# Kernel optimization log

Hardware: AMD Instinct MI355X
Metric: run time of the kernel (lower is better)

The kernel has to match this reference:

```python
import jax, jax.numpy as jnp
import numpy as np

V, N = 3, 32768
C2, C3 = 256, 32          # feat_ch_2D, feat_ch_3D
H = W = 128               # 2D feature map size
D = 32                    # 3D volume feature size
CIN = C2 + C3             # 288, MLP in_channels


def setup_inputs() -> dict:
    key = jax.random.key(0)
    ks = jax.random.split(key, 16)
    sc = 0.02
    inp = {
        'pts': jax.random.uniform(ks[0], (1, N, 3), minval=-0.5, maxval=0.5),
        'pts_proj': jax.random.uniform(ks[1], (1, N, 2), minval=-1.0, maxval=1.0),
        'img_feat0': jax.random.normal(ks[2], (V, C2, H, W)),
        'img_feat1': jax.random.normal(ks[3], (V, C2, H, W)),
        'vol_feat0': jax.random.normal(ks[4], (V, C3, D, D, D)),
        'vol_feat1': jax.random.normal(ks[5], (V, C3, D, D, D)),
        'W0': jax.random.normal(ks[6], (1024, CIN)) * sc,  'b0': jnp.zeros((1024,)),
        'W1': jax.random.normal(ks[7], (512, CIN + 1024)) * sc, 'b1': jnp.zeros((512,)),
        'W2': jax.random.normal(ks[8], (256, CIN + 512)) * sc,  'b2': jnp.zeros((256,)),
        'W3': jax.random.normal(ks[9], (128, CIN + 256)) * sc,  'b3': jnp.zeros((128,)),
        'W4': jax.random.normal(ks[10], (1, 128)) * sc,         'b4': jnp.zeros((1,)),
        'mean_num': 3,
    }
    return inp


def _gs2d(feat, gx, gy):
    # feat: [C,H,W]; gx,gy: [N] normalized coords in [-1,1]
    C, Hh, Ww = feat.shape
    ix = jnp.clip(((gx + 1.0) * Ww - 1.0) * 0.5, 0.0, Ww - 1.0)  # align_corners=False, border pad
    iy = jnp.clip(((gy + 1.0) * Hh - 1.0) * 0.5, 0.0, Hh - 1.0)
    x0f, y0f = jnp.floor(ix), jnp.floor(iy)
    wx, wy = ix - x0f, iy - y0f
    x0 = x0f.astype(jnp.int32); x1 = jnp.minimum(x0 + 1, Ww - 1)
    y0 = y0f.astype(jnp.int32); y1 = jnp.minimum(y0 + 1, Hh - 1)
    v00 = feat[:, y0, x0]; v01 = feat[:, y0, x1]
    v10 = feat[:, y1, x0]; v11 = feat[:, y1, x1]
    return (v00 * (1 - wy) * (1 - wx) + v01 * (1 - wy) * wx
            + v10 * wy * (1 - wx) + v11 * wy * wx)  # [C,N]


def _gs3d(feat, gx, gy, gz):
    # feat: [C,D,H,W]; grid x->W, y->H, z->D (torch grid_sample convention)
    C, Dd, Hh, Ww = feat.shape
    ix = jnp.clip(((gx + 1.0) * Ww - 1.0) * 0.5, 0.0, Ww - 1.0)
    iy = jnp.clip(((gy + 1.0) * Hh - 1.0) * 0.5, 0.0, Hh - 1.0)
    iz = jnp.clip(((gz + 1.0) * Dd - 1.0) * 0.5, 0.0, Dd - 1.0)
    x0f, y0f, z0f = jnp.floor(ix), jnp.floor(iy), jnp.floor(iz)
    wx, wy, wz = ix - x0f, iy - y0f, iz - z0f
    x0 = x0f.astype(jnp.int32); x1 = jnp.minimum(x0 + 1, Ww - 1)
    y0 = y0f.astype(jnp.int32); y1 = jnp.minimum(y0 + 1, Hh - 1)
    z0 = z0f.astype(jnp.int32); z1 = jnp.minimum(z0 + 1, Dd - 1)
    def g(zi, yi, xi):
        return feat[:, zi, yi, xi]  # [C,N]
    out = (g(z0, y0, x0) * (1 - wz) * (1 - wy) * (1 - wx)
           + g(z0, y0, x1) * (1 - wz) * (1 - wy) * wx
           + g(z0, y1, x0) * (1 - wz) * wy * (1 - wx)
           + g(z0, y1, x1) * (1 - wz) * wy * wx
           + g(z1, y0, x0) * wz * (1 - wy) * (1 - wx)
           + g(z1, y0, x1) * wz * (1 - wy) * wx
           + g(z1, y1, x0) * wz * wy * (1 - wx)
           + g(z1, y1, x1) * wz * wy * wx)
    return out  # [C,N]


def _lrelu(x):
    return jnp.where(x >= 0, x, 0.2 * x)


def _conv1x1(Wm, bm, x):
    # x: [V,C,N] -> [V,O,N]
    return jnp.einsum('oc,vcn->von', Wm, x) + bm[None, :, None]


def _mlp0(x, W0, b0, W1, b1, W2, b2, W3, b3):
    out = _lrelu(_conv1x1(W0, b0, x))
    out = _lrelu(_conv1x1(W1, b1, jnp.concatenate([x, out], axis=1)))
    out = _lrelu(_conv1x1(W2, b2, jnp.concatenate([x, out], axis=1)))
    out = _lrelu(_conv1x1(W3, b3, jnp.concatenate([x, out], axis=1)))
    return out  # [V,128,N]


def _forward(pts, pts_proj, img_feats, vol_feats,
             W0, b0, W1, b1, W2, b2, W3, b3, W4, b4, mean_num):
    v = img_feats[0].shape[0]
    gx2 = jnp.broadcast_to(pts_proj[:, :, 0], (v, pts_proj.shape[1]))
    gy2 = jnp.broadcast_to(pts_proj[:, :, 1], (v, pts_proj.shape[1]))
    p = pts * 2.0  # pts *= 2.0 before 3D sampling
    gx3 = jnp.broadcast_to(p[:, :, 0], (v, p.shape[1]))
    gy3 = jnp.broadcast_to(p[:, :, 1], (v, p.shape[1]))
    gz3 = jnp.broadcast_to(p[:, :, 2], (v, p.shape[1]))
    outs = []
    for img_feat, vol_feat in zip(img_feats, vol_feats):
        f2 = jax.vmap(_gs2d)(img_feat, gx2, gy2)            # [V,C2,N]
        f3 = jax.vmap(_gs3d)(vol_feat, gx3, gy3, gz3)       # [V,C3,N]
        pt_feat = jnp.concatenate([f2, f3], axis=1)         # [V,288,N]
        pt_out0 = _mlp0(pt_feat, W0, b0, W1, b1, W2, b2, W3, b3)
        pt_out0_mean = jnp.mean(pt_out0[:mean_num], axis=0, keepdims=True)  # [1,128,N]
        sdf = jax.nn.sigmoid(_conv1x1(W4, b4, pt_out0_mean))                # [1,1,N]
        outs.append(jnp.transpose(sdf, (0, 2, 1)))                          # [1,N,1]
    return tuple(outs)


def reference(pts, pts_proj, img_feat0, img_feat1, vol_feat0, vol_feat1,
              W0, b0, W1, b1, W2, b2, W3, b3, W4, b4, mean_num):
    return _forward(pts, pts_proj, [img_feat0, img_feat1], [vol_feat0, vol_feat1],
                    W0, b0, W1, b1, W2, b2, W3, b3, W4, b4, mean_num)
```

## Files before the change

kernel.cpp:

```cpp
#include <hip/hip_runtime.h>
#include <hip/hip_bf16.h>

#define NV 3
#define NPTS 32768
#define C2C 256
#define C3C 32
#define CINC 288
#define CINP 320
#define HH 128
#define WWW 128
#define DDD 32

typedef short bh8 __attribute__((ext_vector_type(8)));
typedef float fx4 __attribute__((ext_vector_type(4)));
typedef unsigned short us4 __attribute__((ext_vector_type(4)));

__device__ __forceinline__ float b2f(unsigned short u) {
    unsigned int x = ((unsigned int)u) << 16;
    return __uint_as_float(x);
}
__device__ __forceinline__ unsigned short f2b(float f) {
    unsigned int x = __float_as_uint(f);
    unsigned int r = (x + 0x7FFFu + ((x >> 16) & 1u)) >> 16;
    return (unsigned short)r;
}

__device__ __forceinline__ void gl2lds16(const unsigned short* g, unsigned short* l) {
    __builtin_amdgcn_global_load_lds(
        (const __attribute__((address_space(1))) unsigned int*)g,
        (__attribute__((address_space(3))) unsigned int*)l, 16, 0, 0);
}

__device__ __forceinline__ int xcd_swz(int orig, int nwg) {
    int xcd = orig & 7;
    int q = nwg >> 3, r = nwg & 7;
    int base = (xcd < r) ? xcd * (q + 1) : r * (q + 1) + (xcd - r) * q;
    return base + (orig >> 3);
}

__global__ void k_wpad(const float* __restrict__ src, unsigned short* __restrict__ dst, int M, int Kp) {
    int idx = blockIdx.x * 256 + threadIdx.x;
    if (idx >= M * Kp) return;
    int m = idx / Kp, k = idx - m * Kp;
    int Ksrc = Kp - 32;
    float v;
    if (k < CINC) v = src[(size_t)m * Ksrc + k];
    else if (k < CINP) v = 0.0f;
    else v = src[(size_t)m * Ksrc + (k - 32)];
    dst[idx] = f2b(v);
}

__global__ void k_timg(const float* __restrict__ in, unsigned short* __restrict__ out) {
    int v = blockIdx.x >> 7, y = blockIdx.x & 127;
    int x0 = blockIdx.y << 6, c0 = blockIdx.z << 6;
    __shared__ float t[64][65];
    int tx = threadIdx.x & 63, tg = threadIdx.x >> 6;
    const float* src = in + (((size_t)(v * C2C + c0) * HH + y) * WWW + x0);
#pragma unroll
    for (int i = 0; i < 16; i++) {
        int cl = tg * 16 + i;
        t[cl][tx] = src[(size_t)cl * (HH * WWW) + tx];
    }
    __syncthreads();
    unsigned short* dst = out + ((size_t)(v * HH + y) * WWW + x0) * C2C + c0;
#pragma unroll
    for (int i = 0; i < 16; i++) {
        int xl = tg * 16 + i;
        dst[(size_t)xl * C2C + tx] = f2b(t[tx][xl]);
    }
}

__global__ void k_tvol(const float* __restrict__ in, unsigned short* __restrict__ out) {
    int v = blockIdx.x;
    int s0 = blockIdx.y << 8;
    __shared__ float t[32][257];
    int tid = threadIdx.x;
    const float* src = in + (size_t)v * C3C * 32768 + s0;
#pragma unroll
    for (int c = 0; c < 32; c++) t[c][tid] = src[(size_t)c * 32768 + tid];
    __syncthreads();
    unsigned short* dst = out + ((size_t)v * 32768 + s0) * C3C;
    int c = tid & 31, sb = tid >> 5;
#pragma unroll
    for (int j = 0; j < 32; j++) {
        int sl = j * 8 + sb;
        dst[(size_t)sl * C3C + c] = f2b(t[c][sl]);
    }
}

__global__ __launch_bounds__(256) void k_sample(const float* __restrict__ pts, const float* __restrict__ proj,
                         const unsigned short* __restrict__ imgT, const unsigned short* __restrict__ volT,
                         unsigned short* __restrict__ ptT, int n0, int Nk) {
    int w = threadIdx.x >> 6, l = threadIdx.x & 63;
    int i = blockIdx.x * 4 + w;
    int v = blockIdx.y;
    int n = n0 + i;
    unsigned short* dstRow = ptT + (size_t)(v * Nk + i) * CINP;

    {
        float gx = proj[n * 2 + 0], gy = proj[n * 2 + 1];
        float ix = fminf(fmaxf(((gx + 1.0f) * (float)WWW - 1.0f) * 0.5f, 0.0f), (float)(WWW - 1));
        float iy = fminf(fmaxf(((gy + 1.0f) * (float)HH - 1.0f) * 0.5f, 0.0f), (float)(HH - 1));
        float x0f = floorf(ix), y0f = floorf(iy);
        float wx = ix - x0f, wy = iy - y0f;
        int x0 = (int)x0f, y0 = (int)y0f;
        int x1 = min(x0 + 1, WWW - 1), y1 = min(y0 + 1, HH - 1);
        const unsigned short* base = imgT + (size_t)v * HH * WWW * C2C;
        us4 a = *((const us4*)(base + ((size_t)(y0 * WWW + x0)) * C2C) + l);
        us4 b = *((const us4*)(base + ((size_t)(y0 * WWW + x1)) * C2C) + l);
        us4 c = *((const us4*)(base + ((size_t)(y1 * WWW + x0)) * C2C) + l);
        us4 d = *((const us4*)(base + ((size_t)(y1 * WWW + x1)) * C2C) + l);
        float w00 = (1.0f - wy) * (1.0f - wx), w01 = (1.0f - wy) * wx;
        float w10 = wy * (1.0f - wx), w11 = wy * wx;
        us4 rv;
#pragma unroll
        for (int r = 0; r < 4; r++) {
            float f = b2f(a[r]) * w00 + b2f(b[r]) * w01 + b2f(c[r]) * w10 + b2f(d[r]) * w11;
            rv[r] = f2b(f);
        }
        *(us4*)(dstRow + l * 4) = rv;
    }
    {
        float gx = pts[n * 3 + 0] * 2.0f, gy = pts[n * 3 + 1] * 2.0f, gz = pts[n * 3 + 2] * 2.0f;
        float ix = fminf(fmaxf(((gx + 1.0f) * (float)DDD - 1.0f) * 0.5f, 0.0f), (float)(DDD - 1));
        float iy = fminf(fmaxf(((gy + 1.0f) * (float)DDD - 1.0f) * 0.5f, 0.0f), (float)(DDD - 1));
        float iz = fminf(fmaxf(((gz + 1.0f) * (float)DDD - 1.0f) * 0.5f, 0.0f), (float)(DDD - 1));
        float x0f = floorf(ix), y0f = floorf(iy), z0f = floorf(iz);
        float wx = ix - x0f, wy = iy - y0f, wz = iz - z0f;
        int x0 = (int)x0f, y0 = (int)y0f, z0 = (int)z0f;
        int x1 = min(x0 + 1, DDD - 1), y1 = min(y0 + 1, DDD - 1), z1 = min(z0 + 1, DDD - 1);
        int c = l & 31, zs = l >> 5;
        int zi = zs ? z1 : z0;
        float wzs = zs ? wz : (1.0f - wz);
        const unsigned short* base = volT + (size_t)v * 32768 * C3C;
        float f00 = b2f(base[((size_t)((zi * 32 + y0) * 32 + x0)) * C3C + c]);
        float f01 = b2f(base[((size_t)((zi * 32 + y0) * 32 + x1)) * C3C + c]);
        float f10 = b2f(base[((size_t)((zi * 32 + y1) * 32 + x0)) * C3C + c]);
        float f11 = b2f(base[((size_t)((zi * 32 + y1) * 32 + x1)) * C3C + c]);
        float r = (f00 * (1.0f - wy) * (1.0f - wx) + f01 * (1.0f - wy) * wx +
                   f10 * wy * (1.0f - wx) + f11 * wy * wx) * wzs;
        float other = __shfl_xor(r, 32);
        r += other;
        if (zs == 0) dstRow[C2C + c] = f2b(r);
    }
    if (l < 8) *(us4*)(dstRow + CINC + l * 4) = (us4){0, 0, 0, 0};
}

template <int K1, int K2, int M>
__device__ __forceinline__ void gemm128_body(const unsigned short* __restrict__ A,
                                             const unsigned short* __restrict__ B1,
                                             const unsigned short* __restrict__ B2,
                                             const float* __restrict__ bias,
                                             unsigned short* __restrict__ C) {
    constexpr int K = K1 + K2;
    __shared__ unsigned short Ash[128 * 32];
    __shared__ unsigned short Bsh[128 * 32];
    int tid = threadIdx.x;
    int w = tid >> 6, l = tid & 63;
    int la = l & 15, lg = l >> 4;
    int wm = w & 1, wn = w >> 1;
    int gx = gridDim.x;
    int nwg = gx * gridDim.y;
    int bid = xcd_swz(blockIdx.y * gx + blockIdx.x, nwg);
    int mBlk = (bid % gx) * 128;
    int nBlk = (bid / gx) * 128;

    int sRow = l >> 2;
    int sCol = (l & 3) * 8;

    fx4 acc[4][4];
#pragma unroll
    for (int mi = 0; mi < 4; mi++)
#pragma unroll
        for (int ni = 0; ni < 4; ni++) acc[mi][ni] = (fx4){0.f, 0.f, 0.f, 0.f};

    const unsigned short* Ag = A + (size_t)mBlk * K;
    {
        const unsigned short* Bg = B1 + (size_t)nBlk * K1;
        for (int k0 = 0; k0 < K1; k0 += 32) {
#pragma unroll
            for (int j = 0; j < 2; j++) {
                int r = w * 32 + j * 16 + sRow;
                gl2lds16(Ag + (size_t)r * K + k0 + sCol, &Ash[r * 32 + sCol]);
                gl2lds16(Bg + (size_t)r * K1 + k0 + sCol, &Bsh[r * 32 + sCol]);
            }
            __syncthreads();
            bh8 af[4], bfv[4];
#pragma unroll
            for (int mi = 0; mi < 4; mi++) af[mi] = *(const bh8*)&Ash[(wm * 64 + mi * 16 + la) * 32 + lg * 8];
#pragma unroll
            for (int ni = 0; ni < 4; ni++) bfv[ni] = *(const bh8*)&Bsh[(wn * 64 + ni * 16 + la) * 32 + lg * 8];
#pragma unroll
            for (int mi = 0; mi < 4; mi++)
#pragma unroll
                for (int ni = 0; ni < 4; ni++)
                    acc[mi][ni] = __builtin_amdgcn_mfma_f32_16x16x32_bf16(af[mi], bfv[ni], acc[mi][ni], 0, 0, 0);
            __syncthreads();
        }
    }
    if constexpr (K2 > 0) {
        const unsigned short* Bg = B2 + (size_t)nBlk * K2;
        for (int k0 = 0; k0 < K2; k0 += 32) {
#pragma unroll
            for (int j = 0; j < 2; j++) {
                int r = w * 32 + j * 16 + sRow;
                gl2lds16(Ag + (size_t)r * K + K1 + k0 + sCol, &Ash[r * 32 + sCol]);
                gl2lds16(Bg + (size_t)r * K2 + k0 + sCol, &Bsh[r * 32 + sCol]);
            }
            __syncthreads();
            bh8 af[4], bfv[4];
#pragma unroll
            for (int mi = 0; mi < 4; mi++) af[mi] = *(const bh8*)&Ash[(wm * 64 + mi * 16 + la) * 32 + lg * 8];
#pragma unroll
            for (int ni = 0; ni < 4; ni++) bfv[ni] = *(const bh8*)&Bsh[(wn * 64 + ni * 16 + la) * 32 + lg * 8];
#pragma unroll
            for (int mi = 0; mi < 4; mi++)
#pragma unroll
                for (int ni = 0; ni < 4; ni++)
                    acc[mi][ni] = __builtin_amdgcn_mfma_f32_16x16x32_bf16(af[mi], bfv[ni], acc[mi][ni], 0, 0, 0);
            __syncthreads();
        }
    }

#pragma unroll
    for (int mi = 0; mi < 4; mi++) {
        int m0 = mBlk + wm * 64 + mi * 16 + lg * 4;
        fx4 bb = *(const fx4*)(bias + m0);
#pragma unroll
        for (int ni = 0; ni < 4; ni++) {
            int n = nBlk + wn * 64 + ni * 16 + la;
            us4 rv;
#pragma unroll
            for (int r = 0; r < 4; r++) {
                float x = acc[mi][ni][r] + bb[r];
                x = (x >= 0.0f) ? x : 0.2f * x;
                rv[r] = f2b(x);
            }
            *(us4*)(C + (size_t)n * M + m0) = rv;
        }
    }
}

__global__ __launch_bounds__(256) void k_g0(const unsigned short* __restrict__ A, const unsigned short* __restrict__ B1,
                                            const float* __restrict__ bias, unsigned short* __restrict__ C) {
    gemm128_body<320, 0, 1024>(A, B1, nullptr, bias, C);
}
__global__ __launch_bounds__(256) void k_g2(const unsigned short* __restrict__ A, const unsigned short* __restrict__ B1,
                                            const unsigned short* __restrict__ B2, const float* __restrict__ bias,
                                            unsigned short* __restrict__ C) {
    gemm128_body<320, 512, 256>(A, B1, B2, bias, C);
}
__global__ __launch_bounds__(256) void k_g3(const unsigned short* __restrict__ A, const unsigned short* __restrict__ B1,
                                            const unsigned short* __restrict__ B2, const float* __restrict__ bias,
                                            unsigned short* __restrict__ C) {
    gemm128_body<320, 256, 128>(A, B1, B2, bias, C);
}

__global__ __launch_bounds__(512) void k_g1(const unsigned short* __restrict__ A,
                                            const unsigned short* __restrict__ B1,
                                            const unsigned short* __restrict__ B2,
                                            const float* __restrict__ bias,
                                            unsigned short* __restrict__ C, int nOff) {
    constexpr int Kp = 1344;
    constexpr int K2 = 1024;
    constexpr int M = 512;
    constexpr int nt = Kp >> 6;
    __shared__ unsigned short As[2][256 * 64];
    __shared__ unsigned short Bs[2][256 * 64];
    int tid = threadIdx.x;
    int w = tid >> 6, l = tid & 63;
    int la = l & 15, lg = l >> 4;
    int wm = w >> 2, wn = w & 3;
    int gx = gridDim.x;
    int nwg = gx * gridDim.y;
    int bid = xcd_swz(blockIdx.y * gx + blockIdx.x, nwg);
    int mBlk = (bid % gx) * 256;
    int nBlk = (bid / gx) * 256 + nOff;

    const unsigned short* Ag = A + (size_t)mBlk * Kp;

    fx4 acc[8][4];
#pragma unroll
    for (int mi = 0; mi < 8; mi++)
#pragma unroll
        for (int ni = 0; ni < 4; ni++) acc[mi][ni] = (fx4){0.f, 0.f, 0.f, 0.f};

    auto burst = [&](int t, int nxt) {
        const unsigned short* bsrc;
        size_t ldb;
        int kc;
        if (t < 5) { bsrc = B1; ldb = CINP; kc = t * 64; }
        else       { bsrc = B2; ldb = (size_t)K2; kc = (t - 5) * 64; }
        bsrc += (size_t)nBlk * ldb + kc;
        const unsigned short* asrc = Ag + t * 64;
#pragma unroll
        for (int h = 0; h < 2; h++)
#pragma unroll
            for (int j = 0; j < 2; j++) {
                int idx = j * 512 + tid;
                int r = (h << 7) + (idx >> 3);
                int c = (idx & 7) ^ (r & 7);
                gl2lds16(asrc + (size_t)r * Kp + c * 8, &As[nxt][(h << 13) + idx * 8]);
            }
#pragma unroll
        for (int h = 0; h < 2; h++)
#pragma unroll
            for (int j = 0; j < 2; j++) {
                int idx = j * 512 + tid;
                int r = (h << 7) + (idx >> 3);
                int c = (idx & 7) ^ (r & 7);
                gl2lds16(bsrc + (size_t)r * ldb + c * 8, &Bs[nxt][(h << 13) + idx * 8]);
            }
    };

    burst(0, 0);
    asm volatile("s_waitcnt vmcnt(0)" ::: "memory");
    __builtin_amdgcn_s_barrier();
    for (int t = 0; t < nt; t++) {
        int cur = t & 1;
        const unsigned short* Ab = &As[cur][0];
        const unsigned short* Bb = &Bs[cur][0];
        bh8 afr[4][2];
#pragma unroll
        for (int p = 0; p < 4; p++) {
            int qm = p >> 1, qn = p & 1;
            if (qn == 0) {
#pragma unroll
                for (int m2 = 0; m2 < 4; m2++)
#pragma unroll
                    for (int s = 0; s < 2; s++) {
                        int row = wm * 128 + (qm * 4 + m2) * 16 + la;
                        int c = (s * 4 + lg) ^ (row & 7);
                        afr[m2][s] = *(const bh8*)&Ab[row * 64 + c * 8];
                    }
            }
            bh8 bfr[2][2];
#pragma unroll
            for (int n2 = 0; n2 < 2; n2++)
#pragma unroll
                for (int s = 0; s < 2; s++) {
                    int row = wn * 64 + (qn * 2 + n2) * 16 + la;
                    int c = (s * 4 + lg) ^ (row & 7);
                    bfr[n2][s] = *(const bh8*)&Bb[row * 64 + c * 8];
                }
            __builtin_amdgcn_s_barrier();
            __builtin_amdgcn_s_setprio(1);
#pragma unroll
            for (int m2 = 0; m2 < 4; m2++)
#pragma unroll
                for (int n2 = 0; n2 < 2; n2++)
#pragma unroll
                    for (int s = 0; s < 2; s++)
                        acc[qm * 4 + m2][qn * 2 + n2] = __builtin_amdgcn_mfma_f32_16x16x32_bf16(
                            afr[m2][s], bfr[n2][s], acc[qm * 4 + m2][qn * 2 + n2], 0, 0, 0);
            __builtin_amdgcn_s_setprio(0);
            if (p == 0 && t + 1 < nt) burst(t + 1, cur ^ 1);
            if (p == 3) {
                asm volatile("s_waitcnt lgkmcnt(0)" ::: "memory");
                if (t + 1 < nt) asm volatile("s_waitcnt vmcnt(8)" ::: "memory");
            }
            __builtin_amdgcn_s_barrier();
        }
    }

#pragma unroll
    for (int mi = 0; mi < 8; mi++) {
        int m0 = mBlk + wm * 128 + mi * 16 + lg * 4;
        fx4 bb = *(const fx4*)(bias + m0);
#pragma unroll
        for (int ni = 0; ni < 4; ni++) {
            int n = nBlk + wn * 64 + ni * 16 + la;
            us4 rv;
#pragma unroll
            for (int r = 0; r < 4; r++) {
                float x = acc[mi][ni][r] + bb[r];
                x = (x >= 0.0f) ? x : 0.2f * x;
                rv[r] = f2b(x);
            }
            *(us4*)(C + (size_t)n * M + m0) = rv;
        }
    }
}

__global__ __launch_bounds__(256) void k_head(const unsigned short* __restrict__ o3, const float* __restrict__ W4,
                       const float* __restrict__ b4, const int* __restrict__ mn_p,
                       float* __restrict__ out, int n0, int Nk, int level) {
    int wv = threadIdx.x >> 6, l = threadIdx.x & 63;
    int sub = l >> 4, cl = l & 15;
    int i = blockIdx.x * 16 + wv * 4 + sub;
    if (i >= Nk) return;
    int mn = *mn_p;
    if (mn > NV) mn = NV;
    if (mn < 1) mn = 1;
    fx4 w0 = *(const fx4*)(W4 + cl * 8);
    fx4 w1 = *(const fx4*)(W4 + cl * 8 + 4);
    float s = 0.0f;
    for (int v = 0; v < mn; v++) {
        bh8 x = *(const bh8*)(o3 + (size_t)(v * Nk + i) * 128 + cl * 8);
#pragma unroll
        for (int r = 0; r < 4; r++) s += w0[r] * b2f((unsigned short)x[r]);
#pragma unroll
        for (int r = 0; r < 4; r++) s += w1[r] * b2f((unsigned short)x[4 + r]);
    }
#pragma unroll
    for (int m = 1; m < 16; m <<= 1) s += __shfl_xor(s, m);
    if (cl == 0) {
        s = s / (float)mn + b4[0];
        out[(size_t)level * NPTS + n0 + i] = 1.0f / (1.0f + expf(-s));
    }
}

extern "C" void kernel_launch(void* const* d_in, const int* in_sizes, int n_in,
                              void* d_out, int out_size, void* d_ws, size_t ws_size,
                              hipStream_t stream) {
    const float* pts = (const float*)d_in[0];
    const float* proj = (const float*)d_in[1];
    const float* img[2] = {(const float*)d_in[2], (const float*)d_in[3]};
    const float* vol[2] = {(const float*)d_in[4], (const float*)d_in[5]};
    const float* Wf[4] = {(const float*)d_in[6], (const float*)d_in[8], (const float*)d_in[10], (const float*)d_in[12]};
    const float* bf[4] = {(const float*)d_in[7], (const float*)d_in[9], (const float*)d_in[11], (const float*)d_in[13]};
    const float* W4 = (const float*)d_in[14];
    const float* b4 = (const float*)d_in[15];
    const int* mn = (const int*)d_in[16];
    float* out = (float*)d_out;

    const int Kp[4] = {320, 1344, 832, 576};
    const int Msz[4] = {1024, 512, 256, 128};

    char* ws = (char*)d_ws;
    size_t off = 0;
    auto alloc = [&](size_t bytes) -> char* {
        char* p = ws + off;
        off = (off + bytes + 255) & ~(size_t)255;
        return p;
    };

    unsigned short* Wb[4];
    for (int i = 0; i < 4; i++) Wb[i] = (unsigned short*)alloc((size_t)Msz[i] * Kp[i] * 2);
    unsigned short* imgT = (unsigned short*)alloc((size_t)NV * HH * WWW * C2C * 2);
    unsigned short* volT = (unsigned short*)alloc((size_t)NV * 32768 * C3C * 2);
    size_t fixed = off;

    const size_t perPt = (size_t)NV * 2 * (CINP + 1024 + 512 + 256 + 128);
    int Nk = NPTS;
    if (fixed + (size_t)Nk * perPt + 4096 > ws_size) {
        size_t avail = (ws_size > fixed + 4096) ? (ws_size - fixed - 4096) : 0;
        long nk = (long)(avail / perPt);
        nk = (nk / 512) * 512;
        if (nk < 512) nk = 512;
        if (nk > NPTS) nk = NPTS;
        Nk = (int)nk;
    }
    unsigned short* ptT = (unsigned short*)alloc((size_t)NV * Nk * CINP * 2);
    unsigned short* o0 = (unsigned short*)alloc((size_t)NV * Nk * 1024 * 2);
    unsigned short* o1 = (unsigned short*)alloc((size_t)NV * Nk * 512 * 2);
    unsigned short* o2 = (unsigned short*)alloc((size_t)NV * Nk * 256 * 2);
    unsigned short* o3 = (unsigned short*)alloc((size_t)NV * Nk * 128 * 2);

    for (int i = 0; i < 4; i++) {
        int n = Msz[i] * Kp[i];
        k_wpad<<<(n + 255) / 256, 256, 0, stream>>>(Wf[i], Wb[i], Msz[i], Kp[i]);
    }

    for (int lvl = 0; lvl < 2; lvl++) {
        k_timg<<<dim3(NV * HH, WWW / 64, C2C / 64), 256, 0, stream>>>(img[lvl], imgT);
        k_tvol<<<dim3(NV, 32768 / 256), 256, 0, stream>>>(vol[lvl], volT);
        for (int n0 = 0; n0 < NPTS; n0 += Nk) {
            int nk = NPTS - n0 < Nk ? NPTS - n0 : Nk;
            int NC = NV * nk;
            int NH = NC / 2;
            k_sample<<<dim3(nk / 4, NV), 256, 0, stream>>>(pts, proj, imgT, volT, ptT, n0, nk);
            k_g0<<<dim3(1024 / 128, NC / 128), 256, 0, stream>>>(Wb[0], ptT, bf[0], o0);
            k_g1<<<dim3(512 / 256, NH / 256), 512, 0, stream>>>(Wb[1], ptT, o0, bf[1], o1, 0);
            k_g1<<<dim3(512 / 256, NH / 256), 512, 0, stream>>>(Wb[1], ptT, o0, bf[1], o1, NH);
            k_g2<<<dim3(256 / 128, NC / 128), 256, 0, stream>>>(Wb[2], ptT, o1, bf[2], o2);
            k_g3<<<dim3(128 / 128, NC / 128), 256, 0, stream>>>(Wb[3], ptT, o2, bf[3], o3);
            k_head<<<(nk + 15) / 16, 256, 0, stream>>>(o3, W4, b4, mn, out, n0, nk, lvl);
        }
    }
}
```

Measured before the change: 1.089 ms.

## Fuse MLP layers 0 and 1 into one kernel keeping hidden activations in LDS

Replaces the separate layer-0 GEMM and the two layer-1 GEMM launches with a single kernel. Each workgroup loads a 128-point input tile into LDS, computes layer 0 in 128-row chunks, and feeds each activated chunk straight into the layer-1 accumulation through LDS. This removes the 1024-channel intermediate buffer and its global round trip, and lets point chunks grow because workspace per point shrinks. In exchange, weight A-fragments are read directly from global memory without LDS staging or double buffering, there are extra barriers per chunk, and the grid is much smaller with large per-thread accumulator state, which may lower occupancy and MFMA utilisation.

Result: slower. 1.198 ms (+10.0%).

```diff
diff --git a/kernel.cpp b/kernel.cpp
--- a/kernel.cpp
+++ b/kernel.cpp
@@ -146,6 +146,132 @@
     if (l < 8) *(us4*)(dstRow + CINC + l * 4) = (us4){0, 0, 0, 0};
 }
 
+__global__ __launch_bounds__(512) void k_g01(const unsigned short* __restrict__ W0,
+                                             const unsigned short* __restrict__ W1,
+                                             const unsigned short* __restrict__ Bp,
+                                             const float* __restrict__ b0,
+                                             const float* __restrict__ b1,
+                                             unsigned short* __restrict__ C) {
+    __shared__ unsigned short Bt[128 * 320];
+    __shared__ unsigned short Ps[128 * 128];
+    int tid = threadIdx.x;
+    int w = tid >> 6, l = tid & 63;
+    int la = l & 15, lg = l >> 4;
+    int bid = xcd_swz(blockIdx.x, gridDim.x);
+    int nBlk = bid * 128;
+
+    {
+        const unsigned short* src = Bp + (size_t)nBlk * CINP;
+#pragma unroll
+        for (int rnd = 0; rnd < 10; rnd++) {
+            int f = rnd * 512 + tid;
+            int col = f / 40, c = f % 40;
+            int cs = (c & ~7) | ((c & 7) ^ (col & 7));
+            gl2lds16(src + (size_t)col * CINP + cs * 8, &Bt[f * 8]);
+        }
+    }
+    asm volatile("s_waitcnt vmcnt(0)" ::: "memory");
+    __syncthreads();
+
+    fx4 acc[4][8];
+#pragma unroll
+    for (int rf = 0; rf < 4; rf++)
+#pragma unroll
+        for (int cf = 0; cf < 8; cf++) acc[rf][cf] = (fx4){0.f, 0.f, 0.f, 0.f};
+
+    for (int j = 0; j < 8; j++) {
+        fx4 pacc[8];
+#pragma unroll
+        for (int cf = 0; cf < 8; cf++) pacc[cf] = (fx4){0.f, 0.f, 0.f, 0.f};
+        const unsigned short* w0row = W0 + (size_t)(j * 128 + w * 16 + la) * CINP;
+#pragma unroll
+        for (int ks = 0; ks < 10; ks++) {
+            bh8 af = *(const bh8*)(w0row + ks * 32 + lg * 8);
+#pragma unroll
+            for (int cf = 0; cf < 8; cf++) {
+                int col = cf * 16 + la;
+                int c = ks * 4 + lg;
+                int cs = (c & ~7) | ((c & 7) ^ (col & 7));
+                bh8 bfr = *(const bh8*)&Bt[col * CINP + cs * 8];
+                pacc[cf] = __builtin_amdgcn_mfma_f32_16x16x32_bf16(af, bfr, pacc[cf], 0, 0, 0);
+            }
+        }
+        fx4 bb0 = *(const fx4*)(b0 + j * 128 + w * 16 + lg * 4);
+        __syncthreads();
+#pragma unroll
+        for (int cf = 0; cf < 8; cf++) {
+            int col = cf * 16 + la;
+            us4 pv;
+#pragma unroll
+            for (int r = 0; r < 4; r++) {
+                float x = pacc[cf][r] + bb0[r];
+                x = (x >= 0.0f) ? x : 0.2f * x;
+                pv[r] = f2b(x);
+            }
+            int c8 = w * 4 + lg;
+            int cs = (c8 & ~7) | ((c8 & 7) ^ (col & 7));
+            *(us4*)&Ps[col * 128 + cs * 4] = pv;
+        }
+        __syncthreads();
+#pragma unroll
+        for (int ks = 0; ks < 4; ks++) {
+            bh8 af[4];
+#pragma unroll
+            for (int rf = 0; rf < 4; rf++)
+                af[rf] = *(const bh8*)(W1 + (size_t)(w * 64 + rf * 16 + la) * 1344 + CINP + j * 128 + ks * 32 + lg * 8);
+#pragma unroll
+            for (int cf = 0; cf < 8; cf++) {
+                int col = cf * 16 + la;
+                int c8 = ks * 8 + lg * 2;
+                int cs0 = (c8 & ~7) | ((c8 & 7) ^ (col & 7));
+                int cs1 = ((c8 + 1) & ~7) | (((c8 + 1) & 7) ^ (col & 7));
+                us4 lo = *(const us4*)&Ps[col * 128 + cs0 * 4];
+                us4 hi = *(const us4*)&Ps[col * 128 + cs1 * 4];
+                bh8 bfr;
+#pragma unroll
+                for (int r = 0; r < 4; r++) { bfr[r] = (short)lo[r]; bfr[4 + r] = (short)hi[r]; }
+#pragma unroll
+                for (int rf = 0; rf < 4; rf++)
+                    acc[rf][cf] = __builtin_amdgcn_mfma_f32_16x16x32_bf16(af[rf], bfr, acc[rf][cf], 0, 0, 0);
+            }
+        }
+    }
+#pragma unroll
+    for (int ks = 0; ks < 10; ks++) {
+        bh8 af[4];
+#pragma unroll
+        for (int rf = 0; rf < 4; rf++)
+            af[rf] = *(const bh8*)(W1 + (size_t)(w * 64 + rf * 16 + la) * 1344 + ks * 32 + lg * 8);
+#pragma unroll
+        for (int cf = 0; cf < 8; cf++) {
+            int col = cf * 16 + la;
+            int c = ks * 4 + lg;
+            int cs = (c & ~7) | ((c & 7) ^ (col & 7));
+            bh8 bfr = *(const bh8*)&Bt[col * CINP + cs * 8];
+#pragma unroll
+            for (int rf = 0; rf < 4; rf++)
+                acc[rf][cf] = __builtin_amdgcn_mfma_f32_16x16x32_bf16(af[rf], bfr, acc[rf][cf], 0, 0, 0);
+        }
+    }
+#pragma unroll
+    for (int rf = 0; rf < 4; rf++) {
+        int m0 = w * 64 + rf * 16 + lg * 4;
+        fx4 bb = *(const fx4*)(b1 + m0);
+#pragma unroll
+        for (int cf = 0; cf < 8; cf++) {
+            int n = nBlk + cf * 16 + la;
+            us4 rv;
+#pragma unroll
+            for (int r = 0; r < 4; r++) {
+                float x = acc[rf][cf][r] + bb[r];
+                x = (x >= 0.0f) ? x : 0.2f * x;
+                rv[r] = f2b(x);
+            }
+            *(us4*)(C + (size_t)n * 512 + m0) = rv;
+        }
+    }
+}
+
 template <int K1, int K2, int M>
 __device__ __forceinline__ void gemm128_body(const unsigned short* __restrict__ A,
                                              const unsigned short* __restrict__ B1,
@@ -241,10 +367,6 @@
     }
 }
 
-__global__ __launch_bounds__(256) void k_g0(const unsigned short* __restrict__ A, const unsigned short* __restrict__ B1,
-                                            const float* __restrict__ bias, unsigned short* __restrict__ C) {
-    gemm128_body<320, 0, 1024>(A, B1, nullptr, bias, C);
-}
 __global__ __launch_bounds__(256) void k_g2(const unsigned short* __restrict__ A, const unsigned short* __restrict__ B1,
                                             const unsigned short* __restrict__ B2, const float* __restrict__ bias,
                                             unsigned short* __restrict__ C) {
@@ -254,132 +376,6 @@
                                             const unsigned short* __restrict__ B2, const float* __restrict__ bias,
                                             unsigned short* __restrict__ C) {
     gemm128_body<320, 256, 128>(A, B1, B2, bias, C);
-}
-
-__global__ __launch_bounds__(512) void k_g1(const unsigned short* __restrict__ A,
-                                            const unsigned short* __restrict__ B1,
-                                            const unsigned short* __restrict__ B2,
-                                            const float* __restrict__ bias,
-                                            unsigned short* __restrict__ C, int nOff) {
-    constexpr int Kp = 1344;
-    constexpr int K2 = 1024;
-    constexpr int M = 512;
-    constexpr int nt = Kp >> 6;
-    __shared__ unsigned short As[2][256 * 64];
-    __shared__ unsigned short Bs[2][256 * 64];
-    int tid = threadIdx.x;
-    int w = tid >> 6, l = tid & 63;
-    int la = l & 15, lg = l >> 4;
-    int wm = w >> 2, wn = w & 3;
-    int gx = gridDim.x;
-    int nwg = gx * gridDim.y;
-    int bid = xcd_swz(blockIdx.y * gx + blockIdx.x, nwg);
-    int mBlk = (bid % gx) * 256;
-    int nBlk = (bid / gx) * 256 + nOff;
-
-    const unsigned short* Ag = A + (size_t)mBlk * Kp;
-
-    fx4 acc[8][4];
-#pragma unroll
-    for (int mi = 0; mi < 8; mi++)
-#pragma unroll
-        for (int ni = 0; ni < 4; ni++) acc[mi][ni] = (fx4){0.f, 0.f, 0.f, 0.f};
-
-    auto burst = [&](int t, int nxt) {
-        const unsigned short* bsrc;
-        size_t ldb;
-        int kc;
-        if (t < 5) { bsrc = B1; ldb = CINP; kc = t * 64; }
-        else       { bsrc = B2; ldb = (size_t)K2; kc = (t - 5) * 64; }
-        bsrc += (size_t)nBlk * ldb + kc;
-        const unsigned short* asrc = Ag + t * 64;
-#pragma unroll
-        for (int h = 0; h < 2; h++)
-#pragma unroll
-            for (int j = 0; j < 2; j++) {
-                int idx = j * 512 + tid;
-                int r = (h << 7) + (idx >> 3);
-                int c = (idx & 7) ^ (r & 7);
-                gl2lds16(asrc + (size_t)r * Kp + c * 8, &As[nxt][(h << 13) + idx * 8]);
-            }
-#pragma unroll
-        for (int h = 0; h < 2; h++)
-#pragma unroll
-            for (int j = 0; j < 2; j++) {
-                int idx = j * 512 + tid;
-                int r = (h << 7) + (idx >> 3);
-                int c = (idx & 7) ^ (r & 7);
-                gl2lds16(bsrc + (size_t)r * ldb + c * 8, &Bs[nxt][(h << 13) + idx * 8]);
-            }
-    };
-
-    burst(0, 0);
-    asm volatile("s_waitcnt vmcnt(0)" ::: "memory");
-    __builtin_amdgcn_s_barrier();
-    for (int t = 0; t < nt; t++) {
-        int cur = t & 1;
-        const unsigned short* Ab = &As[cur][0];
-        const unsigned short* Bb = &Bs[cur][0];
-        bh8 afr[4][2];
-#pragma unroll
-        for (int p = 0; p < 4; p++) {
-            int qm = p >> 1, qn = p & 1;
-            if (qn == 0) {
-#pragma unroll
-                for (int m2 = 0; m2 < 4; m2++)
-#pragma unroll
-                    for (int s = 0; s < 2; s++) {
-                        int row = wm * 128 + (qm * 4 + m2) * 16 + la;
-                        int c = (s * 4 + lg) ^ (row & 7);
-                        afr[m2][s] = *(const bh8*)&Ab[row * 64 + c * 8];
-                    }
-            }
-            bh8 bfr[2][2];
-#pragma unroll
-            for (int n2 = 0; n2 < 2; n2++)
-#pragma unroll
-                for (int s = 0; s < 2; s++) {
-                    int row = wn * 64 + (qn * 2 + n2) * 16 + la;
-                    int c = (s * 4 + lg) ^ (row & 7);
-                    bfr[n2][s] = *(const bh8*)&Bb[row * 64 + c * 8];
-                }
-            __builtin_amdgcn_s_barrier();
-            __builtin_amdgcn_s_setprio(1);
-#pragma unroll
-            for (int m2 = 0; m2 < 4; m2++)
-#pragma unroll
-                for (int n2 = 0; n2 < 2; n2++)
-#pragma unroll
-                    for (int s = 0; s < 2; s++)
-                        acc[qm * 4 + m2][qn * 2 + n2] = __builtin_amdgcn_mfma_f32_16x16x32_bf16(
-                            afr[m2][s], bfr[n2][s], acc[qm * 4 + m2][qn * 2 + n2], 0, 0, 0);
-            __builtin_amdgcn_s_setprio(0);
-            if (p == 0 && t + 1 < nt) burst(t + 1, cur ^ 1);
-            if (p == 3) {
-                asm volatile("s_waitcnt lgkmcnt(0)" ::: "memory");
-                if (t + 1 < nt) asm volatile("s_waitcnt vmcnt(8)" ::: "memory");
-            }
-            __builtin_amdgcn_s_barrier();
-        }
-    }
-
-#pragma unroll
-    for (int mi = 0; mi < 8; mi++) {
-        int m0 = mBlk + wm * 128 + mi * 16 + lg * 4;
-        fx4 bb = *(const fx4*)(bias + m0);
-#pragma unroll
-        for (int ni = 0; ni < 4; ni++) {
-            int n = nBlk + wn * 64 + ni * 16 + la;
-            us4 rv;
-#pragma unroll
-            for (int r = 0; r < 4; r++) {
-                float x = acc[mi][ni][r] + bb[r];
-                x = (x >= 0.0f) ? x : 0.2f * x;
-                rv[r] = f2b(x);
-            }
-            *(us4*)(C + (size_t)n * M + m0) = rv;
-        }
-    }
 }
 
 __global__ __launch_bounds__(256) void k_head(const unsigned short* __restrict__ o3, const float* __restrict__ W4,
@@ -441,7 +437,7 @@
     unsigned short* volT = (unsigned short*)alloc((size_t)NV * 32768 * C3C * 2);
     size_t fixed = off;
 
-    const size_t perPt = (size_t)NV * 2 * (CINP + 1024 + 512 + 256 + 128);
+    const size_t perPt = (size_t)NV * 2 * (CINP + 512 + 256 + 128);
     int Nk = NPTS;
     if (fixed + (size_t)Nk * perPt + 4096 > ws_size) {
         size_t avail = (ws_size > fixed + 4096) ? (ws_size - fixed - 4096) : 0;
@@ -452,7 +448,6 @@
         Nk = (int)nk;
     }
     unsigned short* ptT = (unsigned short*)alloc((size_t)NV * Nk * CINP * 2);
-    unsigned short* o0 = (unsigned short*)alloc((size_t)NV * Nk * 1024 * 2);
     unsigned short* o1 = (unsigned short*)alloc((size_t)NV * Nk * 512 * 2);
     unsigned short* o2 = (unsigned short*)alloc((size_t)NV * Nk * 256 * 2);
     unsigned short* o3 = (unsigned short*)alloc((size_t)NV * Nk * 128 * 2);
@@ -468,11 +463,8 @@
         for (int n0 = 0; n0 < NPTS; n0 += Nk) {
             int nk = NPTS - n0 < Nk ? NPTS - n0 : Nk;
             int NC = NV * nk;
-            int NH = NC / 2;
             k_sample<<<dim3(nk / 4, NV), 256, 0, stream>>>(pts, proj, imgT, volT, ptT, n0, nk);
-            k_g0<<<dim3(1024 / 128, NC / 128), 256, 0, stream>>>(Wb[0], ptT, bf[0], o0);
-            k_g1<<<dim3(512 / 256, NH / 256), 512, 0, stream>>>(Wb[1], ptT, o0, bf[1], o1, 0);
-            k_g1<<<dim3(512 / 256, NH / 256), 512, 0, stream>>>(Wb[1], ptT, o0, bf[1], o1, NH);
+            k_g01<<<NC / 128, 512, 0, stream>>>(Wb[0], Wb[1], ptT, bf[0], bf[1], o1);
             k_g2<<<dim3(256 / 128, NC / 128), 256, 0, stream>>>(Wb[2], ptT, o1, bf[2], o2);
             k_g3<<<dim3(128 / 128, NC / 128), 256, 0, stream>>>(Wb[3], ptT, o2, bf[3], o3);
             k_head<<<(nk + 15) / 16, 256, 0, stream>>>(o3, W4, b4, mn, out, n0, nk, lvl);
```
